# Kernel tuning notes

Measured on AMD Instinct MI355X. Metric: run time of the kernel, lower is better.

Reference implementation:

```python
import jax, jax.numpy as jnp
import numpy as np

N = 50000          # nodes
E = 400000         # edges (avg degree 8)
KER_IN = 6         # edge attr dim: (x_i, x_j, a_i, a_j) in 2D
W = 16             # node channel width
KW = 128           # kernel MLP hidden width
DEPTH = 4


def setup_inputs() -> dict:
    key = jax.random.key(0)
    ks = jax.random.split(key, 12)
    p = lambda k, shape, fan_in: (jax.random.normal(k, shape, jnp.float32) / np.sqrt(fan_in)).astype(jnp.float32)
    return {
        "x": jax.random.normal(ks[0], (N, 1), jnp.float32),
        "edge_index": jax.random.randint(ks[1], (2, E), 0, N, dtype=jnp.int32).astype(jnp.int64),
        "edge_attr": jax.random.uniform(ks[2], (E, KER_IN), jnp.float32),
        # fc1: in_width=1 -> width
        "fc1_w": p(ks[3], (1, W), 1), "fc1_b": jnp.zeros((W,), jnp.float32),
        # kernel DenseNet [6,128,128,256], ReLU between layers, linear last
        "k1_w": p(ks[4], (KER_IN, KW), KER_IN), "k1_b": jnp.zeros((KW,), jnp.float32),
        "k2_w": p(ks[5], (KW, KW), KW), "k2_b": jnp.zeros((KW,), jnp.float32),
        "k3_w": p(ks[6], (KW, W * W), KW), "k3_b": jnp.zeros((W * W,), jnp.float32),
        # NNConv_old root weight and bias
        "root_w": p(ks[7], (W, W), W), "conv_b": jnp.zeros((W,), jnp.float32),
        # fc2: width -> 1
        "fc2_w": p(ks[8], (W, 1), W), "fc2_b": jnp.zeros((1,), jnp.float32),
    }


def reference(x, edge_index, edge_attr, fc1_w, fc1_b, k1_w, k1_b, k2_w, k2_b,
              k3_w, k3_b, root_w, conv_b, fc2_w, fc2_b):
    src, dst = edge_index[0], edge_index[1]
    n = x.shape[0]
    e = edge_attr.shape[0]
    # Per-edge kernel weights depend only on edge_attr -> compute once (same
    # math as recomputing inside the depth loop, since conv1 is reused).
    h = jax.nn.relu(edge_attr @ k1_w + k1_b)        # [E, KW]
    h = jax.nn.relu(h @ k2_w + k2_b)                # [E, KW]
    Wk = (h @ k3_w + k3_b).reshape(e, W, W)         # [E, W, W]
    # Mean-aggregation denominator (0-in-degree nodes stay zero via max(.,1)).
    deg = jax.ops.segment_sum(jnp.ones((e,), jnp.float32), dst, num_segments=n)
    deg = jnp.maximum(deg, 1.0)[:, None]            # [N, 1]

    feat = x @ fc1_w + fc1_b                        # [N, W]
    for _ in range(DEPTH):
        msg = jnp.einsum('ei,eio->eo', feat[src], Wk)              # [E, W]
        agg = jax.ops.segment_sum(msg, dst, num_segments=n) / deg  # [N, W] scatter-mean
        feat = jax.nn.relu(agg + feat @ root_w + conv_b)
    return feat @ fc2_w + fc2_b                     # [N, 1]
```

## Files before the change

kernel.cpp:

```cpp
#include <hip/hip_runtime.h>
#include <stdint.h>

typedef __attribute__((ext_vector_type(8))) short short8;
typedef __attribute__((ext_vector_type(4))) float f32x4;

static __device__ __forceinline__ uint16_t f2bf(float f) {
  uint32_t u = __builtin_bit_cast(uint32_t, f);
  u += 0x7FFFu + ((u >> 16) & 1u);
  return (uint16_t)(u >> 16);
}

__global__ __launch_bounds__(256) void k_zeroi(int* __restrict__ p, int n) {
  int i = blockIdx.x * 256 + threadIdx.x;
  if (i < n) p[i] = 0;
}
__global__ __launch_bounds__(256) void k_copyi(const int* __restrict__ a,
                                               int* __restrict__ b, int n) {
  int i = blockIdx.x * 256 + threadIdx.x;
  if (i < n) b[i] = a[i];
}

__global__ __launch_bounds__(256) void k_detect(const long long* ei64, int n64,
                                                long long nmax, int* flag) {
  __shared__ int ok;
  if (threadIdx.x == 0) ok = 1;
  __syncthreads();
  for (int i = threadIdx.x; i < n64; i += 256) {
    long long v = ei64[i];
    if (v < 0 || v >= nmax) atomicAnd(&ok, 0);
  }
  __syncthreads();
  if (threadIdx.x == 0) *flag = ok;
}

__global__ __launch_bounds__(256) void k_convert(const void* ei, int e2,
                                                 const int* __restrict__ flag,
                                                 int* __restrict__ out) {
  int i = blockIdx.x * 256 + threadIdx.x;
  if (i >= e2) return;
  out[i] = (*flag) ? (int)((const long long*)ei)[i] : ((const int*)ei)[i];
}

__global__ __launch_bounds__(256) void k_count(const int* __restrict__ dst, int E,
                                               int* __restrict__ cnt) {
  int i = blockIdx.x * 256 + threadIdx.x;
  if (i < E) atomicAdd(&cnt[dst[i]], 1);
}

__global__ __launch_bounds__(256) void k_scan1(const int* __restrict__ cnt, int n,
                                               int* __restrict__ excl,
                                               int* __restrict__ bsum) {
  __shared__ int s[256];
  int i = blockIdx.x * 256 + threadIdx.x;
  int v = (i < n) ? cnt[i] : 0;
  s[threadIdx.x] = v;
  __syncthreads();
  #pragma unroll
  for (int off = 1; off < 256; off <<= 1) {
    int t = (threadIdx.x >= off) ? s[threadIdx.x - off] : 0;
    __syncthreads();
    s[threadIdx.x] += t;
    __syncthreads();
  }
  if (i < n) excl[i] = s[threadIdx.x] - v;
  if (threadIdx.x == 255) bsum[blockIdx.x] = s[255];
}
__global__ void k_scan2(int* bsum, int nb) {
  if (threadIdx.x == 0 && blockIdx.x == 0) {
    int run = 0;
    for (int b = 0; b < nb; ++b) { int t = bsum[b]; bsum[b] = run; run += t; }
  }
}
__global__ __launch_bounds__(256) void k_scan3(int* __restrict__ excl,
                                               const int* __restrict__ bsum,
                                               int n, int E) {
  int i = blockIdx.x * 256 + threadIdx.x;
  if (i < n) excl[i] += bsum[blockIdx.x];
  if (i == 0) excl[n] = E;
}

__global__ __launch_bounds__(256) void k_scatter(const int* __restrict__ src,
                                                 const int* __restrict__ dst, int E,
                                                 int* __restrict__ rowcur,
                                                 int* __restrict__ eid,
                                                 int* __restrict__ srcS) {
  int e = blockIdx.x * 256 + threadIdx.x;
  if (e >= E) return;
  int d = dst[e];
  int pos = atomicAdd(&rowcur[d], 1);
  eid[pos] = e;
  srcS[pos] = src[e];
}

__global__ __launch_bounds__(256) void k_prep(const float* __restrict__ k2w,
                                              const float* __restrict__ k3w,
                                              uint16_t* __restrict__ w2t,
                                              uint16_t* __restrict__ w3t) {
  int d = blockIdx.x * 256 + threadIdx.x;
  int tile = d >> 9, ww = d & 511;
  int m16 = ww >> 5, q4 = (ww >> 3) & 3, jj = ww & 7;
  int ot = tile >> 2, kst = tile & 3;
  int k = kst * 32 + q4 * 8 + jj;
  if (d < 16384) {
    int j = ot * 16 + m16;
    w2t[d] = f2bf(k2w[k * 128 + j]);
  }
  if (d < 32768) {
    int oc = ot * 16 + m16;
    w3t[d] = f2bf(k3w[k * 256 + oc]);
  }
}

__global__ __launch_bounds__(256) void k_feat0(const float* __restrict__ x,
                                               const float* __restrict__ w,
                                               const float* __restrict__ b,
                                               float* __restrict__ feat, int N) {
  int n = blockIdx.x * 256 + threadIdx.x;
  if (n >= N) return;
  float xv = x[n];
  float4* fp = (float4*)(feat + (size_t)n * 16);
  #pragma unroll
  for (int q = 0; q < 4; ++q) {
    float4 v;
    v.x = xv * w[q*4+0] + b[q*4+0];
    v.y = xv * w[q*4+1] + b[q*4+1];
    v.z = xv * w[q*4+2] + b[q*4+2];
    v.w = xv * w[q*4+3] + b[q*4+3];
    fp[q] = v;
  }
}

__global__ __launch_bounds__(256) void k_mlp12(
    const float* __restrict__ ea, const int* __restrict__ eid,
    const float* __restrict__ k1w, const float* __restrict__ k1b,
    const uint16_t* __restrict__ w2t, const float* __restrict__ k2b,
    uint16_t* __restrict__ h2, int e0, int e1) {
  __shared__ uint16_t s_w2[16384];
  __shared__ float s_k1[768];
  __shared__ float s_b1[128];
  __shared__ float s_b2[128];
  int tid = threadIdx.x;
  #pragma unroll
  for (int it = 0; it < 8; ++it) {
    int g = it * 256 + tid;
    int tile = g >> 6, o8 = g & 63;
    ((uint4*)s_w2)[tile * 64 + (o8 & 3) * 16 + (o8 >> 2)] = ((const uint4*)w2t)[g];
  }
  for (int i = tid; i < 768; i += 256) s_k1[i] = k1w[i];
  if (tid < 128) { s_b1[tid] = k1b[tid]; s_b2[tid] = k2b[tid]; }
  __syncthreads();

  int w = tid >> 6, lane = tid & 63;
  int m16 = lane & 15, q4 = lane >> 4;
  int wbase = e0 + blockIdx.x * 256 + w * 64;

  #pragma unroll
  for (int et = 0; et < 4; ++et) {
    int i0 = wbase + et * 16;
    int i = i0 + m16;
    int ic = i < e1 ? i : e1 - 1;
    int es = eid[ic];
    const float* ap = ea + (size_t)es * 6;
    float a0 = ap[0], a1 = ap[1], a2 = ap[2], a3 = ap[3], a4 = ap[4], a5 = ap[5];

    short8 Y[4];
    #pragma unroll
    for (int kst = 0; kst < 4; ++kst) {
      short8 y;
      #pragma unroll
      for (int jj = 0; jj < 8; ++jj) {
        int k = kst*32 + q4*8 + jj;
        float v = s_b1[k] + a0*s_k1[k] + a1*s_k1[128+k] + a2*s_k1[256+k]
                + a3*s_k1[384+k] + a4*s_k1[512+k] + a5*s_k1[640+k];
        v = fmaxf(v, 0.0f);
        y[jj] = (short)f2bf(v);
      }
      Y[kst] = y;
    }

    f32x4 acc[8];
    #pragma unroll
    for (int jt = 0; jt < 8; ++jt) acc[jt] = f32x4{0.f,0.f,0.f,0.f};
    #pragma unroll
    for (int kst = 0; kst < 4; ++kst) {
      #pragma unroll
      for (int jt = 0; jt < 8; ++jt) {
        short8 X = *(const short8*)&s_w2[(jt*4 + kst)*512 + lane*8];
        acc[jt] = __builtin_amdgcn_mfma_f32_16x16x32_bf16(X, Y[kst], acc[jt], 0, 0, 0);
      }
    }

    if (i < e1) {
      size_t hb = (size_t)((i0 - e0) >> 4) * 2048;
      #pragma unroll
      for (int jt = 0; jt < 8; ++jt) {
        int jb = jt*16 + q4*4;
        float v0 = fmaxf(acc[jt][0] + s_b2[jb+0], 0.0f);
        float v1 = fmaxf(acc[jt][1] + s_b2[jb+1], 0.0f);
        float v2 = fmaxf(acc[jt][2] + s_b2[jb+2], 0.0f);
        float v3 = fmaxf(acc[jt][3] + s_b2[jb+3], 0.0f);
        uint2 pk;
        pk.x = ((uint32_t)f2bf(v1) << 16) | f2bf(v0);
        pk.y = ((uint32_t)f2bf(v3) << 16) | f2bf(v2);
        size_t off = hb + (size_t)(((jt*2 + (q4>>1))*16 + m16)*8 + (q4&1)*4);
        *(uint2*)&h2[off] = pk;
      }
    }
  }
}

__global__ __launch_bounds__(256) void k_fused(
    const uint16_t* __restrict__ h2, const uint16_t* __restrict__ w3t,
    const float* __restrict__ k3b, const float* __restrict__ feat,
    const int* __restrict__ srcS, float* __restrict__ msg, int e0, int e1) {
  __shared__ uint16_t s_w3[32768];
  __shared__ float s_b3[256];
  int tid = threadIdx.x;
  #pragma unroll
  for (int it = 0; it < 16; ++it) {
    int g = it * 256 + tid;
    int tile = g >> 6, o8 = g & 63;
    ((uint4*)s_w3)[tile * 64 + (o8 & 3) * 16 + (o8 >> 2)] = ((const uint4*)w3t)[g];
  }
  s_b3[tid] = k3b[tid];
  __syncthreads();

  int w = tid >> 6, lane = tid & 63;
  int m16 = lane & 15, q4 = lane >> 4;
  int wbase = e0 + blockIdx.x * 256 + w * 64;
  int maxt = (e1 - 1 - e0) >> 4;

  short8 Yc[4], Yn[4];
  {
    int t = (wbase - e0) >> 4; if (t > maxt) t = maxt;
    const uint16_t* hb = h2 + (size_t)t * 2048;
    #pragma unroll
    for (int kst = 0; kst < 4; ++kst)
      Yc[kst] = *(const short8*)&hb[(size_t)((kst*4 + q4)*16 + m16)*8];
  }

  #pragma unroll
  for (int et = 0; et < 4; ++et) {
    int i0 = wbase + et * 16;
    int i = i0 + m16;
    int ic = i < e1 ? i : e1 - 1;
    int s = srcS[ic];
    const float4* fp = (const float4*)(feat + (size_t)s * 16);
    float4 f0 = fp[0], f1 = fp[1], f2 = fp[2], f3 = fp[3];

    if (et < 3) {
      int t = ((wbase - e0) >> 4) + et + 1; if (t > maxt) t = maxt;
      const uint16_t* hb = h2 + (size_t)t * 2048;
      #pragma unroll
      for (int kst = 0; kst < 4; ++kst)
        Yn[kst] = *(const short8*)&hb[(size_t)((kst*4 + q4)*16 + m16)*8];
    }

    f32x4 acc[16];
    #pragma unroll
    for (int t = 0; t < 16; ++t) acc[t] = f32x4{0.f,0.f,0.f,0.f};
    #pragma unroll
    for (int kst = 0; kst < 4; ++kst) {
      #pragma unroll
      for (int oct = 0; oct < 16; ++oct) {
        short8 X = *(const short8*)&s_w3[(oct*4 + kst)*512 + lane*8];
        acc[oct] = __builtin_amdgcn_mfma_f32_16x16x32_bf16(X, Yc[kst], acc[oct], 0, 0, 0);
      }
    }

    float f[16] = {f0.x, f0.y, f0.z, f0.w, f1.x, f1.y, f1.z, f1.w,
                   f2.x, f2.y, f2.z, f2.w, f3.x, f3.y, f3.z, f3.w};
    float4 m = {0.f, 0.f, 0.f, 0.f};
    #pragma unroll
    for (int ii = 0; ii < 16; ++ii) {
      float4 bv = *(const float4*)&s_b3[ii*16 + q4*4];
      float fi = f[ii];
      m.x += fi * (acc[ii][0] + bv.x);
      m.y += fi * (acc[ii][1] + bv.y);
      m.z += fi * (acc[ii][2] + bv.z);
      m.w += fi * (acc[ii][3] + bv.w);
    }
    if (i < e1) *(float4*)(msg + (size_t)i * 16 + q4 * 4) = m;

    #pragma unroll
    for (int kst = 0; kst < 4; ++kst) Yc[kst] = Yn[kst];
  }
}

__global__ __launch_bounds__(256) void k_agg(
    const float* __restrict__ msg, const int* __restrict__ rowptr,
    const float* __restrict__ fin, const float* __restrict__ rootw,
    const float* __restrict__ convb, float* __restrict__ fout, int N) {
  __shared__ float s_rw[256];
  __shared__ float s_cb[16];
  int tid = threadIdx.x;
  s_rw[tid] = rootw[tid];
  if (tid < 16) s_cb[tid] = convb[tid];
  __syncthreads();
  int n = blockIdx.x * 16 + (tid >> 4);
  int ch = tid & 15;
  if (n >= N) return;
  int p0 = rowptr[n], p1 = rowptr[n+1];
  float sum = 0.0f;
  for (int p = p0; p < p1; ++p) sum += msg[(size_t)p * 16 + ch];
  float di = 1.0f / fmaxf((float)(p1 - p0), 1.0f);
  float o = s_cb[ch] + sum * di;
  const float* fp = fin + (size_t)n * 16;
  #pragma unroll
  for (int i = 0; i < 16; ++i) o += fp[i] * s_rw[i*16 + ch];
  fout[(size_t)n * 16 + ch] = fmaxf(o, 0.0f);
}

__global__ __launch_bounds__(256) void k_out(const float* __restrict__ feat,
                                             const float* __restrict__ w,
                                             const float* __restrict__ b,
                                             float* __restrict__ out, int N) {
  int n = blockIdx.x * 256 + threadIdx.x;
  if (n >= N) return;
  const float4* fp = (const float4*)(feat + (size_t)n*16);
  float acc = b[0];
  #pragma unroll
  for (int q = 0; q < 4; ++q) {
    float4 t = fp[q];
    acc += t.x*w[q*4] + t.y*w[q*4+1] + t.z*w[q*4+2] + t.w*w[q*4+3];
  }
  out[n] = acc;
}

extern "C" void kernel_launch(void* const* d_in, const int* in_sizes, int n_in,
                              void* d_out, int out_size, void* d_ws, size_t ws_size,
                              hipStream_t stream) {
  const float* x     = (const float*)d_in[0];
  const void*  ei    = d_in[1];
  const float* ea    = (const float*)d_in[2];
  const float* fc1w  = (const float*)d_in[3];
  const float* fc1b  = (const float*)d_in[4];
  const float* k1w   = (const float*)d_in[5];
  const float* k1b   = (const float*)d_in[6];
  const float* k2w   = (const float*)d_in[7];
  const float* k2b   = (const float*)d_in[8];
  const float* k3w   = (const float*)d_in[9];
  const float* k3b   = (const float*)d_in[10];
  const float* rootw = (const float*)d_in[11];
  const float* convb = (const float*)d_in[12];
  const float* fc2w  = (const float*)d_in[13];
  const float* fc2b  = (const float*)d_in[14];
  int N = in_sizes[0];
  int E = in_sizes[1] / 2;

  char* base = (char*)d_ws;
  size_t off = 0;
  auto alloc = [&](size_t bytes) -> void* {
    void* p = base + off;
    off = (off + bytes + 255) & ~(size_t)255;
    return p;
  };
  int*      idx    = (int*)alloc((size_t)2*E*sizeof(int));
  int*      flag   = (int*)alloc(256);
  int*      rowptr = (int*)alloc((size_t)(N+1)*sizeof(int));
  int*      rowcur = (int*)alloc((size_t)N*sizeof(int));
  int*      bsum   = (int*)alloc(1024*sizeof(int));
  int*      eid    = (int*)alloc((size_t)E*sizeof(int));
  int*      srcS   = (int*)alloc((size_t)E*sizeof(int));
  float*    fA     = (float*)alloc((size_t)N*16*sizeof(float));
  float*    fB     = (float*)alloc((size_t)N*16*sizeof(float));
  float*    msg    = (float*)alloc((size_t)E*16*sizeof(float));
  uint16_t* w2t    = (uint16_t*)alloc(16384*2);
  uint16_t* w3t    = (uint16_t*)alloc(32768*2);
  if (off > ws_size) return;

  long long avail = (long long)ws_size - (long long)off;
  long long fullBytes = (long long)E * 256;
  int chunkE;
  if (avail >= fullBytes) {
    chunkE = E;
  } else {
    chunkE = (int)((avail / 256) & ~511LL);
    if (chunkE < 512) chunkE = 512;
  }
  uint16_t* h2 = (uint16_t*)alloc((size_t)chunkE * 256);
  bool full = (chunkE >= E);

  int* srcI = idx;
  int* dstI = idx + E;

  int n64 = E < 1024 ? E : 1024;
  k_detect<<<1, 256, 0, stream>>>((const long long*)ei, n64, (long long)N, flag);
  k_convert<<<(2*E + 255)/256, 256, 0, stream>>>(ei, 2*E, flag, idx);

  int nbN = (N + 255) / 256;
  k_zeroi<<<nbN, 256, 0, stream>>>(rowcur, N);
  k_count<<<(E + 255)/256, 256, 0, stream>>>(dstI, E, rowcur);
  k_scan1<<<nbN, 256, 0, stream>>>(rowcur, N, rowptr, bsum);
  k_scan2<<<1, 64, 0, stream>>>(bsum, nbN);
  k_scan3<<<nbN, 256, 0, stream>>>(rowptr, bsum, N, E);
  k_copyi<<<nbN, 256, 0, stream>>>(rowptr, rowcur, N);
  k_scatter<<<(E + 255)/256, 256, 0, stream>>>(srcI, dstI, E, rowcur, eid, srcS);

  k_prep<<<128, 256, 0, stream>>>(k2w, k3w, w2t, w3t);
  k_feat0<<<(N + 255)/256, 256, 0, stream>>>(x, fc1w, fc1b, fA, N);
  if (full)
    k_mlp12<<<(E + 255)/256, 256, 0, stream>>>(ea, eid, k1w, k1b, w2t, k2b, h2, 0, E);

  float* fin = fA;
  float* fout = fB;
  int nbAgg = (N + 15) / 16;
  for (int d = 0; d < 4; ++d) {
    if (full) {
      k_fused<<<(E + 255)/256, 256, 0, stream>>>(h2, w3t, k3b, fin, srcS, msg, 0, E);
    } else {
      for (int i0 = 0; i0 < E; i0 += chunkE) {
        int i1 = i0 + chunkE < E ? i0 + chunkE : E;
        k_mlp12<<<(i1 - i0 + 255)/256, 256, 0, stream>>>(ea, eid, k1w, k1b, w2t, k2b, h2, i0, i1);
        k_fused<<<(i1 - i0 + 255)/256, 256, 0, stream>>>(h2, w3t, k3b, fin, srcS, msg, i0, i1);
      }
    }
    k_agg<<<nbAgg, 256, 0, stream>>>(msg, rowptr, fin, rootw, convb, fout, N);
    float* t = fin; fin = fout; fout = t;
  }
  k_out<<<(N + 255)/256, 256, 0, stream>>>(fin, fc2w, fc2b, (float*)d_out, N);
}
```

Before: 461.6 us.

## Process two edge tiles per wave concurrently in fused kernel, halve edges per block

Each wave in k_fused now handles 32 edges as two 16-edge tiles at once instead of 64 edges as four tiles in sequence. Every LDS load of a w3 fragment feeds two independent MFMA chains, and all operand and feature loads are issued up front. The grid doubles to keep total coverage. The aim is more instruction-level parallelism and less LDS traffic per MFMA. In exchange the kernel holds twice the accumulator registers, and the 64KB w3 staging into LDS is repeated per block over twice as many blocks.

```diff
diff --git a/kernel.cpp b/kernel.cpp
--- a/kernel.cpp
+++ b/kernel.cpp
@@ -227,63 +227,62 @@
 
   int w = tid >> 6, lane = tid & 63;
   int m16 = lane & 15, q4 = lane >> 4;
-  int wbase = e0 + blockIdx.x * 256 + w * 64;
+  int wbase = e0 + blockIdx.x * 128 + w * 32;
   int maxt = (e1 - 1 - e0) >> 4;
 
-  short8 Yc[4], Yn[4];
-  {
-    int t = (wbase - e0) >> 4; if (t > maxt) t = maxt;
+  short8 Y[2][4];
+  #pragma unroll
+  for (int et = 0; et < 2; ++et) {
+    int t = ((wbase - e0) >> 4) + et; if (t > maxt) t = maxt;
     const uint16_t* hb = h2 + (size_t)t * 2048;
     #pragma unroll
     for (int kst = 0; kst < 4; ++kst)
-      Yc[kst] = *(const short8*)&hb[(size_t)((kst*4 + q4)*16 + m16)*8];
-  }
-
-  #pragma unroll
-  for (int et = 0; et < 4; ++et) {
-    int i0 = wbase + et * 16;
-    int i = i0 + m16;
+      Y[et][kst] = *(const short8*)&hb[(size_t)((kst*4 + q4)*16 + m16)*8];
+  }
+
+  float f[2][16];
+  #pragma unroll
+  for (int et = 0; et < 2; ++et) {
+    int i = wbase + et*16 + m16;
     int ic = i < e1 ? i : e1 - 1;
     int s = srcS[ic];
     const float4* fp = (const float4*)(feat + (size_t)s * 16);
-    float4 f0 = fp[0], f1 = fp[1], f2 = fp[2], f3 = fp[3];
-
-    if (et < 3) {
-      int t = ((wbase - e0) >> 4) + et + 1; if (t > maxt) t = maxt;
-      const uint16_t* hb = h2 + (size_t)t * 2048;
-      #pragma unroll
-      for (int kst = 0; kst < 4; ++kst)
-        Yn[kst] = *(const short8*)&hb[(size_t)((kst*4 + q4)*16 + m16)*8];
-    }
-
-    f32x4 acc[16];
-    #pragma unroll
-    for (int t = 0; t < 16; ++t) acc[t] = f32x4{0.f,0.f,0.f,0.f};
-    #pragma unroll
-    for (int kst = 0; kst < 4; ++kst) {
-      #pragma unroll
-      for (int oct = 0; oct < 16; ++oct) {
-        short8 X = *(const short8*)&s_w3[(oct*4 + kst)*512 + lane*8];
-        acc[oct] = __builtin_amdgcn_mfma_f32_16x16x32_bf16(X, Yc[kst], acc[oct], 0, 0, 0);
-      }
-    }
-
-    float f[16] = {f0.x, f0.y, f0.z, f0.w, f1.x, f1.y, f1.z, f1.w,
-                   f2.x, f2.y, f2.z, f2.w, f3.x, f3.y, f3.z, f3.w};
+    #pragma unroll
+    for (int q = 0; q < 4; ++q) {
+      float4 t = fp[q];
+      f[et][q*4] = t.x; f[et][q*4+1] = t.y; f[et][q*4+2] = t.z; f[et][q*4+3] = t.w;
+    }
+  }
+
+  f32x4 acc[2][16];
+  #pragma unroll
+  for (int et = 0; et < 2; ++et)
+    #pragma unroll
+    for (int t = 0; t < 16; ++t) acc[et][t] = f32x4{0.f,0.f,0.f,0.f};
+  #pragma unroll
+  for (int kst = 0; kst < 4; ++kst) {
+    #pragma unroll
+    for (int oct = 0; oct < 16; ++oct) {
+      short8 X = *(const short8*)&s_w3[(oct*4 + kst)*512 + lane*8];
+      acc[0][oct] = __builtin_amdgcn_mfma_f32_16x16x32_bf16(X, Y[0][kst], acc[0][oct], 0, 0, 0);
+      acc[1][oct] = __builtin_amdgcn_mfma_f32_16x16x32_bf16(X, Y[1][kst], acc[1][oct], 0, 0, 0);
+    }
+  }
+
+  #pragma unroll
+  for (int et = 0; et < 2; ++et) {
     float4 m = {0.f, 0.f, 0.f, 0.f};
     #pragma unroll
     for (int ii = 0; ii < 16; ++ii) {
       float4 bv = *(const float4*)&s_b3[ii*16 + q4*4];
-      float fi = f[ii];
-      m.x += fi * (acc[ii][0] + bv.x);
-      m.y += fi * (acc[ii][1] + bv.y);
-      m.z += fi * (acc[ii][2] + bv.z);
-      m.w += fi * (acc[ii][3] + bv.w);
-    }
+      float fi = f[et][ii];
+      m.x += fi * (acc[et][ii][0] + bv.x);
+      m.y += fi * (acc[et][ii][1] + bv.y);
+      m.z += fi * (acc[et][ii][2] + bv.z);
+      m.w += fi * (acc[et][ii][3] + bv.w);
+    }
+    int i = wbase + et*16 + m16;
     if (i < e1) *(float4*)(msg + (size_t)i * 16 + q4 * 4) = m;
-
-    #pragma unroll
-    for (int kst = 0; kst < 4; ++kst) Yc[kst] = Yn[kst];
   }
 }
 
@@ -407,12 +406,12 @@
   int nbAgg = (N + 15) / 16;
   for (int d = 0; d < 4; ++d) {
     if (full) {
-      k_fused<<<(E + 255)/256, 256, 0, stream>>>(h2, w3t, k3b, fin, srcS, msg, 0, E);
+      k_fused<<<(E + 127)/128, 256, 0, stream>>>(h2, w3t, k3b, fin, srcS, msg, 0, E);
     } else {
       for (int i0 = 0; i0 < E; i0 += chunkE) {
         int i1 = i0 + chunkE < E ? i0 + chunkE : E;
         k_mlp12<<<(i1 - i0 + 255)/256, 256, 0, stream>>>(ea, eid, k1w, k1b, w2t, k2b, h2, i0, i1);
-        k_fused<<<(i1 - i0 + 255)/256, 256, 0, stream>>>(h2, w3t, k3b, fin, srcS, msg, i0, i1);
+        k_fused<<<(i1 - i0 + 127)/128, 256, 0, stream>>>(h2, w3t, k3b, fin, srcS, msg, i0, i1);
       }
     }
     k_agg<<<nbAgg, 256, 0, stream>>>(msg, rowptr, fin, rootw, convb, fout, N);
```

After: 508.4 us. 1.1x slower.
